# Optimization experiments

Measured on AMD Instinct MI355X. Metric: run time of the kernel, lower is better.

Reference implementation:

```python
import jax, jax.numpy as jnp
import numpy as np


def setup_inputs() -> dict:
    key = jax.random.key(0)
    k1, k2, k3 = jax.random.split(key, 3)
    B, D_IN, HIDDEN = 4096, 1024, 32768  # hidden = d_in * scale_size(32)
    x = jax.random.normal(k1, (B, D_IN), dtype=jnp.float32)
    W_enc = jax.random.normal(k2, (HIDDEN, D_IN), dtype=jnp.float32) * (1.0 / np.sqrt(D_IN))
    b_enc = jnp.zeros((HIDDEN,), dtype=jnp.float32)  # encoder.bias.data.zero_()
    # W_dec = encoder.weight.clone() then unit-norm rows (set_decoder_norm_to_unit_norm)
    W_dec = jax.random.normal(k3, (HIDDEN, D_IN), dtype=jnp.float32)
    W_dec = W_dec / (jnp.linalg.norm(W_dec, axis=1, keepdims=True) + jnp.finfo(jnp.float32).eps)
    b_dec = jnp.zeros((D_IN,), dtype=jnp.float32)
    return {"x": x, "W_enc": W_enc, "b_enc": b_enc, "W_dec": W_dec, "b_dec": b_dec, "k": 32}


def reference(x, W_enc, b_enc, W_dec, b_dec, k):
    # sae_in = x - b_dec; pre_acts = relu(encoder(sae_in))
    sae_in = x - b_dec
    pre_acts = jax.nn.relu(jnp.einsum('bd,hd->bh', sae_in, W_enc) + b_enc)  # [B, H]
    # topk_activation: keep top-k per row, zero elsewhere, then z @ W_dec.
    # Equivalent sparse decode: gather the k rows of W_dec and contract.
    topk_vals, topk_idx = jax.lax.top_k(pre_acts, k)  # [B, k]
    # x_reconstructed = z @ W_dec + b_dec  (z is the dense scatter of topk)
    x_rec = jnp.einsum('bk,bkd->bd', topk_vals, W_dec[topk_idx]) + b_dec
    return x_rec
```

## Files before the change

### kernel.cpp

```cpp
#include <hip/hip_runtime.h>
#include <hip/hip_bf16.h>
#include <stdint.h>
#include <stddef.h>


#define BROWS 4096
#define DIN   1024
#define HID   32768
#define KTOP  32
#define KC    48
#define PT    16

#define BM 256
#define BN 256
#define BK 64
#define NT (DIN / BK)
#define EP 264

typedef short short8_t __attribute__((ext_vector_type(8)));
typedef float fx4 __attribute__((ext_vector_type(4)));

__device__ __forceinline__ unsigned short f2bf(float f) {
  unsigned u = __float_as_uint(f);
  u += 0x7FFFu + ((u >> 16) & 1u);
  return (unsigned short)(u >> 16);
}

__global__ __launch_bounds__(256) void conv_wc(const float* __restrict__ W,
                                               unsigned short* __restrict__ Wbc, int c0) {
  int base = (blockIdx.x * 256 + threadIdx.x) * 4;
  float4 v = *(const float4*)(W + (size_t)c0 * DIN + base);
  ushort4 o;
  o.x = f2bf(v.x); o.y = f2bf(v.y); o.z = f2bf(v.z); o.w = f2bf(v.w);
  *(ushort4*)(Wbc + base) = o;
}

__global__ __launch_bounds__(256) void prep_x(const float* __restrict__ x,
                                              const float* __restrict__ bdec,
                                              unsigned short* __restrict__ xbf) {
  int base = (blockIdx.x * 256 + threadIdx.x) * 4;
  int col = base & (DIN - 1);
  float4 xv = *(const float4*)(x + base);
  float4 bv = *(const float4*)(bdec + col);
  ushort4 o;
  o.x = f2bf(xv.x - bv.x); o.y = f2bf(xv.y - bv.y);
  o.z = f2bf(xv.z - bv.z); o.w = f2bf(xv.w - bv.w);
  *(ushort4*)(xbf + base) = o;
}

__global__ __launch_bounds__(256) void init_cand(unsigned* __restrict__ cand) {
  int i = blockIdx.x * 256 + threadIdx.x;
  if (i < BROWS * KC) cand[i] = 0u;
}


__device__ __forceinline__ void stage_half(const unsigned short* __restrict__ g0,
                                           unsigned short* l0, int t, int k0) {
  const int w6 = (t >> 6) << 6;
#pragma unroll
  for (int i = 0; i < 2; ++i) {
    const int l  = i * 512 + t;
    const int r  = l >> 3;
    const int cl = (l & 7) ^ (r & 7);
    const unsigned short* g = g0 + (size_t)r * DIN + k0 + cl * 8;
    unsigned short* ld = l0 + (size_t)(i * 512 + w6) * 8;
    __builtin_amdgcn_global_load_lds((const __attribute__((address_space(1))) unsigned int*)g,
                                     (__attribute__((address_space(3))) unsigned int*)ld,
                                     16, 0, 0);
  }
}

__device__ __forceinline__ void tile_step(int tt,
                                          const unsigned short* __restrict__ Ab,
                                          const unsigned short* __restrict__ Wb,
                                          unsigned short* bc, unsigned short* bn,
                                          fx4 (&acc)[8][4],
                                          int t, int l16, int quad, int wm, int wn) {
  const int k1 = (tt + 1) * BK;
  const int k2 = (tt + 2) * BK;
  if (tt < NT - 1) { asm volatile("s_waitcnt vmcnt(4)" ::: "memory"); }
  else             { asm volatile("s_waitcnt vmcnt(0)" ::: "memory"); }
  __builtin_amdgcn_s_barrier();

  const unsigned short* Ar = bc + wm * 8192;
  const unsigned short* Br = bc + 16384 + (wn * 64 + l16) * 64;
  const int xs = l16 & 7;
  short8_t a[8], b0, b1;

#pragma unroll
  for (int mt = 0; mt < 8; ++mt)
    a[mt] = *(const short8_t*)(Ar + (mt * 16 + l16) * 64 + ((quad ^ xs) * 8));
  b0 = *(const short8_t*)(Br + 0 * 1024 + ((quad ^ xs) * 8));
  b1 = *(const short8_t*)(Br + 1 * 1024 + ((quad ^ xs) * 8));
  if (tt + 1 < NT) stage_half(Wb, bn + 16384, t, k1);
  __builtin_amdgcn_s_barrier();
  __builtin_amdgcn_s_setprio(1);
#pragma unroll
  for (int mt = 0; mt < 8; ++mt)
    acc[mt][0] = __builtin_amdgcn_mfma_f32_16x16x32_bf16(a[mt], b0, acc[mt][0], 0, 0, 0);
#pragma unroll
  for (int mt = 0; mt < 8; ++mt)
    acc[mt][1] = __builtin_amdgcn_mfma_f32_16x16x32_bf16(a[mt], b1, acc[mt][1], 0, 0, 0);
  __builtin_amdgcn_s_setprio(0);
  __builtin_amdgcn_s_barrier();

  b0 = *(const short8_t*)(Br + 2 * 1024 + ((quad ^ xs) * 8));
  b1 = *(const short8_t*)(Br + 3 * 1024 + ((quad ^ xs) * 8));
  if (tt + 1 < NT) stage_half(Wb + 128 * DIN, bn + 24576, t, k1);
  __builtin_amdgcn_s_barrier();
  __builtin_amdgcn_s_setprio(1);
#pragma unroll
  for (int mt = 0; mt < 8; ++mt)
    acc[mt][2] = __builtin_amdgcn_mfma_f32_16x16x32_bf16(a[mt], b0, acc[mt][2], 0, 0, 0);
#pragma unroll
  for (int mt = 0; mt < 8; ++mt)
    acc[mt][3] = __builtin_amdgcn_mfma_f32_16x16x32_bf16(a[mt], b1, acc[mt][3], 0, 0, 0);
  __builtin_amdgcn_s_setprio(0);
  __builtin_amdgcn_s_barrier();

#pragma unroll
  for (int mt = 0; mt < 8; ++mt)
    a[mt] = *(const short8_t*)(Ar + (mt * 16 + l16) * 64 + (((4 + quad) ^ xs) * 8));
  b0 = *(const short8_t*)(Br + 0 * 1024 + (((4 + quad) ^ xs) * 8));
  b1 = *(const short8_t*)(Br + 1 * 1024 + (((4 + quad) ^ xs) * 8));
  __builtin_amdgcn_s_barrier();
  __builtin_amdgcn_s_setprio(1);
#pragma unroll
  for (int mt = 0; mt < 8; ++mt)
    acc[mt][0] = __builtin_amdgcn_mfma_f32_16x16x32_bf16(a[mt], b0, acc[mt][0], 0, 0, 0);
#pragma unroll
  for (int mt = 0; mt < 8; ++mt)
    acc[mt][1] = __builtin_amdgcn_mfma_f32_16x16x32_bf16(a[mt], b1, acc[mt][1], 0, 0, 0);
  __builtin_amdgcn_s_setprio(0);
  __builtin_amdgcn_s_barrier();

  b0 = *(const short8_t*)(Br + 2 * 1024 + (((4 + quad) ^ xs) * 8));
  b1 = *(const short8_t*)(Br + 3 * 1024 + (((4 + quad) ^ xs) * 8));
  if (tt + 2 < NT) {
    stage_half(Ab,             bc,        t, k2);
    stage_half(Ab + 128 * DIN, bc + 8192, t, k2);
  }
  __builtin_amdgcn_s_barrier();
  __builtin_amdgcn_s_setprio(1);
#pragma unroll
  for (int mt = 0; mt < 8; ++mt)
    acc[mt][2] = __builtin_amdgcn_mfma_f32_16x16x32_bf16(a[mt], b0, acc[mt][2], 0, 0, 0);
#pragma unroll
  for (int mt = 0; mt < 8; ++mt)
    acc[mt][3] = __builtin_amdgcn_mfma_f32_16x16x32_bf16(a[mt], b1, acc[mt][3], 0, 0, 0);
  __builtin_amdgcn_s_setprio(0);
  __builtin_amdgcn_s_barrier();
}

__global__ __launch_bounds__(512, 2) void gemm_scores(
    const unsigned short* __restrict__ A,
    const unsigned short* __restrict__ W,
    const float* __restrict__ benc,
    unsigned short* __restrict__ scores,
    int Hc, int c0) {
  extern __shared__ unsigned short lds[];
  const int t    = threadIdx.x;
  const int lane = t & 63;
  const int wv   = t >> 6;
  const int wm   = wv >> 2;
  const int wn   = wv & 3;
  const int l16  = lane & 15;
  const int quad = lane >> 4;

  const int nwg  = (int)(gridDim.x * gridDim.y);
  const int orig = (int)(blockIdx.y * gridDim.x + blockIdx.x);
  const int q    = nwg >> 3, r8 = nwg & 7;
  const int xcd  = orig & 7, loc = orig >> 3;
  const int swz  = (xcd < r8 ? xcd * (q + 1) : r8 * (q + 1) + (xcd - r8) * q) + loc;
  const int bx   = swz % (int)gridDim.x;
  const int by   = swz / (int)gridDim.x;

  const int row0  = by * BM;
  const int colc0 = bx * BN;
  const unsigned short* Ab = A + (size_t)row0 * DIN;
  const unsigned short* Wb = W + (size_t)colc0 * DIN;

  unsigned short* buf0 = lds;
  unsigned short* buf1 = lds + 32768;

  fx4 acc[8][4];
  fx4 zero = {0.f, 0.f, 0.f, 0.f};
#pragma unroll
  for (int i = 0; i < 8; ++i)
#pragma unroll
    for (int j = 0; j < 4; ++j) acc[i][j] = zero;

  stage_half(Ab,            buf0,         t, 0);
  stage_half(Ab + 128*DIN,  buf0 + 8192,  t, 0);
  stage_half(Wb,            buf0 + 16384, t, 0);
  stage_half(Wb + 128*DIN,  buf0 + 24576, t, 0);
  stage_half(Ab,            buf1,         t, BK);
  stage_half(Ab + 128*DIN,  buf1 + 8192,  t, BK);

#pragma unroll 1
  for (int it = 0; it < NT / 2; ++it) {
    tile_step(2 * it,     Ab, Wb, buf0, buf1, acc, t, l16, quad, wm, wn);
    tile_step(2 * it + 1, Ab, Wb, buf1, buf0, acc, t, l16, quad, wm, wn);
  }

  const int colbase = colc0 + wn * 64;
  float bval[4];
#pragma unroll
  for (int nt = 0; nt < 4; ++nt) bval[nt] = benc[c0 + colbase + nt * 16 + l16];

  unsigned short* et = lds;
#pragma unroll
  for (int c = 0; c < 2; ++c) {
    __syncthreads();
    if (wm == c) {
#pragma unroll
      for (int nt = 0; nt < 4; ++nt) {
        const int col = wn * 64 + nt * 16 + l16;
#pragma unroll
        for (int mt = 0; mt < 8; ++mt)
#pragma unroll
          for (int rg = 0; rg < 4; ++rg) {
            const int row = mt * 16 + quad * 4 + rg;
            float v = acc[mt][nt][rg] + bval[nt];
            et[row * EP + col] = f2bf(v > 0.f ? v : 0.f);
          }
      }
    }
    __syncthreads();
    {
      const int row = t >> 2;
      const size_t gro = (size_t)(row0 + c * 128 + row) * Hc + colc0;
#pragma unroll
      for (int i = 0; i < 8; ++i) {
        const int ch = (t & 3) * 8 + i;
        short8_t v = *(const short8_t*)(et + row * EP + ch * 8);
        *(short8_t*)(scores + gro + ch * 8) = v;
      }
    }
  }
}

__global__ __launch_bounds__(128) void topk_cand(const unsigned short* __restrict__ scores,
                                                 int Hc, int c0,
                                                 unsigned* __restrict__ cand) {
  __shared__ unsigned lk[128 * 17];
  const int row = blockIdx.x;
  const int t = threadIdx.x;
  unsigned s[PT];
#pragma unroll
  for (int j = 0; j < PT; ++j) s[j] = 0u;

  const unsigned short* srow = scores + (size_t)row * Hc;
  for (int cb = t * 8; cb < Hc; cb += 128 * 8) {
    short8_t v = *(const short8_t*)(srow + cb);
    int gcb = c0 + cb;
#pragma unroll
    for (int e = 0; e < 8; ++e) {
      unsigned val = (unsigned)(unsigned short)v[e];
      unsigned key = (val << 16) | (unsigned)(0x7FFF - (gcb + e));
      if (key > s[PT - 1]) {
        unsigned prev = 0xFFFFFFFFu;
#pragma unroll
        for (int j = 0; j < PT; ++j) {
          unsigned sj = s[j];
          s[j] = (sj >= key) ? sj : (prev < key ? prev : key);
          prev = sj;
        }
      }
    }
  }
  if (t < KC) {
    unsigned key = cand[row * KC + t];
    if (key > s[PT - 1]) {
      unsigned prev = 0xFFFFFFFFu;
#pragma unroll
      for (int j = 0; j < PT; ++j) {
        unsigned sj = s[j];
        s[j] = (sj >= key) ? sj : (prev < key ? prev : key);
        prev = sj;
      }
    }
  }
#pragma unroll
  for (int j = 0; j < PT; ++j) lk[t * 17 + j] = s[j];
  __syncthreads();

  if (t < 64) {
    unsigned k0 = lk[t * 17];
    unsigned k1 = lk[(t + 64) * 17];
    int h0 = 0, h1 = 0;
    unsigned mywin = 0;
    for (int it = 0; it < KC; ++it) {
      unsigned wmax = (k0 > k1) ? k0 : k1;
#pragma unroll
      for (int off = 32; off >= 1; off >>= 1) {
        unsigned o = __shfl_down(wmax, (unsigned)off);
        if (o > wmax) wmax = o;
      }
      wmax = __shfl(wmax, 0);
      if (it == t) mywin = wmax;
      if (k0 == wmax)      { ++h0; k0 = (h0 < PT) ? lk[t * 17 + h0] : 0u; }
      else if (k1 == wmax) { ++h1; k1 = (h1 < PT) ? lk[(t + 64) * 17 + h1] : 0u; }
    }
    if (t < KC) cand[row * KC + t] = mywin;
  }
}

__global__ __launch_bounds__(256) void rescore_decode(
    const unsigned* __restrict__ cand,
    const float* __restrict__ x, const float* __restrict__ Wenc,
    const float* __restrict__ benc,
    const float* __restrict__ Wdec, const float* __restrict__ bdec,
    float* __restrict__ out) {
  __shared__ float xr[DIN];
  __shared__ double sc[KC];
  __shared__ int   scol[KC];
  __shared__ float fv[KTOP];
  __shared__ int   fi[KTOP];
  const int row = blockIdx.x, t = threadIdx.x;

  {
    float4 xv = *(const float4*)(x + (size_t)row * DIN + t * 4);
    float4 bv = *(const float4*)(bdec + t * 4);
    *(float4*)(xr + t * 4) = make_float4(xv.x - bv.x, xv.y - bv.y, xv.z - bv.z, xv.w - bv.w);
  }
  if (t < KC) scol[t] = 0x7FFF - (int)(cand[row * KC + t] & 0xFFFFu);
  if (t < KTOP) { fv[t] = 0.f; fi[t] = 0; }
  __syncthreads();

  const int wave = t >> 6, lane = t & 63;
  for (int j = wave; j < KC; j += 4) {
    int col = scol[j];
    const float* wr = Wenc + (size_t)col * DIN;
    double p = 0.0;
#pragma unroll
    for (int q = 0; q < 4; ++q) {
      int o = q * 256 + lane * 4;
      float4 w = *(const float4*)(wr + o);
      float4 xv = *(const float4*)(xr + o);
      p += (double)xv.x * (double)w.x + (double)xv.y * (double)w.y +
           (double)xv.z * (double)w.z + (double)xv.w * (double)w.w;
    }
#pragma unroll
    for (int off = 32; off >= 1; off >>= 1) p += __shfl_down(p, off);
    if (lane == 0) {
      double v = p + (double)benc[col];
      sc[j] = v > 0.0 ? v : 0.0;
    }
  }
  __syncthreads();

  if (t < KC) {
    double mv = sc[t];
    int mc = scol[t];
    int rank = 0;
    for (int j = 0; j < KC; ++j) {
      double oj = sc[j];
      if (oj > mv || (oj == mv && (scol[j] < mc || (scol[j] == mc && j < t)))) ++rank;
    }
    if (rank < KTOP) { fv[rank] = (float)mv; fi[rank] = mc; }
  }
  __syncthreads();

  const int c = t * 4;
  float4 bd = *(const float4*)(bdec + c);
  float a0 = bd.x, a1 = bd.y, a2 = bd.z, a3 = bd.w;
#pragma unroll 8
  for (int j = 0; j < KTOP; ++j) {
    float v = fv[j];
    float4 w = *(const float4*)(Wdec + (size_t)fi[j] * DIN + c);
    a0 += v * w.x; a1 += v * w.y; a2 += v * w.z; a3 += v * w.w;
  }
  *(float4*)(out + (size_t)row * DIN + c) = make_float4(a0, a1, a2, a3);
}

extern "C" void kernel_launch(void* const* d_in, const int* in_sizes, int n_in,
                              void* d_out, int out_size, void* d_ws, size_t ws_size,
                              hipStream_t stream) {
  const float* x    = (const float*)d_in[0];
  const float* Wenc = (const float*)d_in[1];
  const float* benc = (const float*)d_in[2];
  const float* Wdec = (const float*)d_in[3];
  const float* bdec = (const float*)d_in[4];
  float* out = (float*)d_out;

  char* ws = (char*)d_ws;
  unsigned short* xbf  = (unsigned short*)ws;
  unsigned*       cand = (unsigned*)(ws + (8u << 20));

  const size_t fixed = (size_t)(9u << 20);
  int Hc = HID;
  while (Hc > 256 &&
         fixed + (size_t)Hc * DIN * 2 + (size_t)BROWS * Hc * 2 > ws_size)
    Hc >>= 1;

  unsigned short* Wbc    = (unsigned short*)(ws + fixed);
  unsigned short* scores = (unsigned short*)(ws + fixed + (size_t)Hc * DIN * 2);

  static bool attr_set = false;
  if (!attr_set) {
    (void)hipFuncSetAttribute((const void*)gemm_scores,
                              hipFuncAttributeMaxDynamicSharedMemorySize, 131072);
    attr_set = true;
  }

  prep_x<<<BROWS * DIN / 1024, 256, 0, stream>>>(x, bdec, xbf);
  init_cand<<<(BROWS * KC + 255) / 256, 256, 0, stream>>>(cand);
  for (int c0 = 0; c0 < HID; c0 += Hc) {
    conv_wc<<<Hc, 256, 0, stream>>>(Wenc, Wbc, c0);
    gemm_scores<<<dim3(Hc / BN, BROWS / BM), 512, 131072, stream>>>(xbf, Wbc, benc, scores, Hc, c0);
    topk_cand<<<BROWS, 128, 0, stream>>>(scores, Hc, c0, cand);
  }
  rescore_decode<<<BROWS, 256, 0, stream>>>(cand, x, Wenc, benc, Wdec, bdec, out);
}
```

Baseline: 1.020 ms.

## Restructure GEMM tile step into 2x2 register-blocked MFMA quadrants with fewer barriers

```diff
diff --git a/kernel.cpp b/kernel.cpp
--- a/kernel.cpp
+++ b/kernel.cpp
@@ -54,20 +54,14 @@
 }
 
 
-__device__ __forceinline__ void stage_half(const unsigned short* __restrict__ g0,
-                                           unsigned short* l0, int t, int k0) {
-  const int w6 = (t >> 6) << 6;
-#pragma unroll
-  for (int i = 0; i < 2; ++i) {
-    const int l  = i * 512 + t;
-    const int r  = l >> 3;
-    const int cl = (l & 7) ^ (r & 7);
-    const unsigned short* g = g0 + (size_t)r * DIN + k0 + cl * 8;
-    unsigned short* ld = l0 + (size_t)(i * 512 + w6) * 8;
-    __builtin_amdgcn_global_load_lds((const __attribute__((address_space(1))) unsigned int*)g,
-                                     (__attribute__((address_space(3))) unsigned int*)ld,
-                                     16, 0, 0);
-  }
+__device__ __forceinline__ void stage_pair(const unsigned short* __restrict__ g,
+                                           unsigned short* l0, int voff, int w8) {
+  __builtin_amdgcn_global_load_lds((const __attribute__((address_space(1))) unsigned int*)(g + voff),
+                                   (__attribute__((address_space(3))) unsigned int*)(l0 + w8),
+                                   16, 0, 0);
+  __builtin_amdgcn_global_load_lds((const __attribute__((address_space(1))) unsigned int*)(g + voff + 64 * DIN),
+                                   (__attribute__((address_space(3))) unsigned int*)(l0 + w8 + 4096),
+                                   16, 0, 0);
 }
 
 __device__ __forceinline__ void tile_step(int tt,
@@ -75,81 +69,68 @@
                                           const unsigned short* __restrict__ Wb,
                                           unsigned short* bc, unsigned short* bn,
                                           fx4 (&acc)[8][4],
-                                          int t, int l16, int quad, int wm, int wn) {
-  const int k1 = (tt + 1) * BK;
-  const int k2 = (tt + 2) * BK;
+                                          int voff, int w8, int l16, int quad, int wm, int wn) {
   if (tt < NT - 1) { asm volatile("s_waitcnt vmcnt(4)" ::: "memory"); }
   else             { asm volatile("s_waitcnt vmcnt(0)" ::: "memory"); }
   __builtin_amdgcn_s_barrier();
 
-  const unsigned short* Ar = bc + wm * 8192;
+  const unsigned short* Ar = bc + wm * 8192 + l16 * 64;
   const unsigned short* Br = bc + 16384 + (wn * 64 + l16) * 64;
   const int xs = l16 & 7;
-  short8_t a[8], b0, b1;
-
-#pragma unroll
-  for (int mt = 0; mt < 8; ++mt)
-    a[mt] = *(const short8_t*)(Ar + (mt * 16 + l16) * 64 + ((quad ^ xs) * 8));
-  b0 = *(const short8_t*)(Br + 0 * 1024 + ((quad ^ xs) * 8));
-  b1 = *(const short8_t*)(Br + 1 * 1024 + ((quad ^ xs) * 8));
-  if (tt + 1 < NT) stage_half(Wb, bn + 16384, t, k1);
+  const int o0 = (quad ^ xs) * 8;
+  const int o1 = ((4 + quad) ^ xs) * 8;
+
+  short8_t aP[4], aQ[4], bP[4], bQ[4];
+#pragma unroll
+  for (int i = 0; i < 4; ++i) aP[i] = *(const short8_t*)(Ar + i * 1024 + o0);
+#pragma unroll
+  for (int i = 0; i < 4; ++i) bP[i] = *(const short8_t*)(Br + i * 1024 + o0);
+  if (tt + 1 < NT) {
+    stage_pair(Wb + (tt + 1) * BK,             bn + 16384, voff, w8);
+    stage_pair(Wb + 128 * DIN + (tt + 1) * BK, bn + 24576, voff, w8);
+  }
+#pragma unroll
+  for (int i = 0; i < 4; ++i) aQ[i] = *(const short8_t*)(Ar + (4 + i) * 1024 + o0);
+  __builtin_amdgcn_s_setprio(1);
+#pragma unroll
+  for (int i = 0; i < 4; ++i)
+#pragma unroll
+    for (int nt = 0; nt < 4; ++nt)
+      acc[i][nt] = __builtin_amdgcn_mfma_f32_16x16x32_bf16(aP[i], bP[nt], acc[i][nt], 0, 0, 0);
+  __builtin_amdgcn_s_setprio(0);
+
+#pragma unroll
+  for (int i = 0; i < 4; ++i) aP[i] = *(const short8_t*)(Ar + i * 1024 + o1);
+#pragma unroll
+  for (int i = 0; i < 4; ++i) bQ[i] = *(const short8_t*)(Br + i * 1024 + o1);
+  __builtin_amdgcn_s_setprio(1);
+#pragma unroll
+  for (int i = 0; i < 4; ++i)
+#pragma unroll
+    for (int nt = 0; nt < 4; ++nt)
+      acc[4 + i][nt] = __builtin_amdgcn_mfma_f32_16x16x32_bf16(aQ[i], bP[nt], acc[4 + i][nt], 0, 0, 0);
+  __builtin_amdgcn_s_setprio(0);
+
+#pragma unroll
+  for (int i = 0; i < 4; ++i) aQ[i] = *(const short8_t*)(Ar + (4 + i) * 1024 + o1);
+  __builtin_amdgcn_s_setprio(1);
+#pragma unroll
+  for (int i = 0; i < 4; ++i)
+#pragma unroll
+    for (int nt = 0; nt < 4; ++nt)
+      acc[i][nt] = __builtin_amdgcn_mfma_f32_16x16x32_bf16(aP[i], bQ[nt], acc[i][nt], 0, 0, 0);
+#pragma unroll
+  for (int i = 0; i < 4; ++i)
+#pragma unroll
+    for (int nt = 0; nt < 4; ++nt)
+      acc[4 + i][nt] = __builtin_amdgcn_mfma_f32_16x16x32_bf16(aQ[i], bQ[nt], acc[4 + i][nt], 0, 0, 0);
+  __builtin_amdgcn_s_setprio(0);
+
   __builtin_amdgcn_s_barrier();
-  __builtin_amdgcn_s_setprio(1);
-#pragma unroll
-  for (int mt = 0; mt < 8; ++mt)
-    acc[mt][0] = __builtin_amdgcn_mfma_f32_16x16x32_bf16(a[mt], b0, acc[mt][0], 0, 0, 0);
-#pragma unroll
-  for (int mt = 0; mt < 8; ++mt)
-    acc[mt][1] = __builtin_amdgcn_mfma_f32_16x16x32_bf16(a[mt], b1, acc[mt][1], 0, 0, 0);
-  __builtin_amdgcn_s_setprio(0);
-  __builtin_amdgcn_s_barrier();
-
-  b0 = *(const short8_t*)(Br + 2 * 1024 + ((quad ^ xs) * 8));
-  b1 = *(const short8_t*)(Br + 3 * 1024 + ((quad ^ xs) * 8));
-  if (tt + 1 < NT) stage_half(Wb + 128 * DIN, bn + 24576, t, k1);
-  __builtin_amdgcn_s_barrier();
-  __builtin_amdgcn_s_setprio(1);
-#pragma unroll
-  for (int mt = 0; mt < 8; ++mt)
-    acc[mt][2] = __builtin_amdgcn_mfma_f32_16x16x32_bf16(a[mt], b0, acc[mt][2], 0, 0, 0);
-#pragma unroll
-  for (int mt = 0; mt < 8; ++mt)
-    acc[mt][3] = __builtin_amdgcn_mfma_f32_16x16x32_bf16(a[mt], b1, acc[mt][3], 0, 0, 0);
-  __builtin_amdgcn_s_setprio(0);
-  __builtin_amdgcn_s_barrier();
-
-#pragma unroll
-  for (int mt = 0; mt < 8; ++mt)
-    a[mt] = *(const short8_t*)(Ar + (mt * 16 + l16) * 64 + (((4 + quad) ^ xs) * 8));
-  b0 = *(const short8_t*)(Br + 0 * 1024 + (((4 + quad) ^ xs) * 8));
-  b1 = *(const short8_t*)(Br + 1 * 1024 + (((4 + quad) ^ xs) * 8));
-  __builtin_amdgcn_s_barrier();
-  __builtin_amdgcn_s_setprio(1);
-#pragma unroll
-  for (int mt = 0; mt < 8; ++mt)
-    acc[mt][0] = __builtin_amdgcn_mfma_f32_16x16x32_bf16(a[mt], b0, acc[mt][0], 0, 0, 0);
-#pragma unroll
-  for (int mt = 0; mt < 8; ++mt)
-    acc[mt][1] = __builtin_amdgcn_mfma_f32_16x16x32_bf16(a[mt], b1, acc[mt][1], 0, 0, 0);
-  __builtin_amdgcn_s_setprio(0);
-  __builtin_amdgcn_s_barrier();
-
-  b0 = *(const short8_t*)(Br + 2 * 1024 + (((4 + quad) ^ xs) * 8));
-  b1 = *(const short8_t*)(Br + 3 * 1024 + (((4 + quad) ^ xs) * 8));
   if (tt + 2 < NT) {
-    stage_half(Ab,             bc,        t, k2);
-    stage_half(Ab + 128 * DIN, bc + 8192, t, k2);
-  }
-  __builtin_amdgcn_s_barrier();
-  __builtin_amdgcn_s_setprio(1);
-#pragma unroll
-  for (int mt = 0; mt < 8; ++mt)
-    acc[mt][2] = __builtin_amdgcn_mfma_f32_16x16x32_bf16(a[mt], b0, acc[mt][2], 0, 0, 0);
-#pragma unroll
-  for (int mt = 0; mt < 8; ++mt)
-    acc[mt][3] = __builtin_amdgcn_mfma_f32_16x16x32_bf16(a[mt], b1, acc[mt][3], 0, 0, 0);
-  __builtin_amdgcn_s_setprio(0);
-  __builtin_amdgcn_s_barrier();
+    stage_pair(Ab + (tt + 2) * BK,             bc,        voff, w8);
+    stage_pair(Ab + 128 * DIN + (tt + 2) * BK, bc + 8192, voff, w8);
+  }
 }
 
 __global__ __launch_bounds__(512, 2) void gemm_scores(
@@ -167,13 +148,14 @@
   const int l16  = lane & 15;
   const int quad = lane >> 4;
 
-  const int nwg  = (int)(gridDim.x * gridDim.y);
-  const int orig = (int)(blockIdx.y * gridDim.x + blockIdx.x);
+  const int gx   = (int)gridDim.x, gy = (int)gridDim.y;
+  const int nwg  = gx * gy;
+  const int orig = (int)blockIdx.x * gy + (int)blockIdx.y;
   const int q    = nwg >> 3, r8 = nwg & 7;
   const int xcd  = orig & 7, loc = orig >> 3;
   const int swz  = (xcd < r8 ? xcd * (q + 1) : r8 * (q + 1) + (xcd - r8) * q) + loc;
-  const int bx   = swz % (int)gridDim.x;
-  const int by   = swz / (int)gridDim.x;
+  const int bx   = swz / gy;
+  const int by   = swz % gy;
 
   const int row0  = by * BM;
   const int colc0 = bx * BN;
@@ -183,6 +165,10 @@
   unsigned short* buf0 = lds;
   unsigned short* buf1 = lds + 32768;
 
+  const int r_   = t >> 3;
+  const int voff = r_ * DIN + ((t & 7) ^ (r_ & 7)) * 8;
+  const int w8   = (t & ~63) * 8;
+
   fx4 acc[8][4];
   fx4 zero = {0.f, 0.f, 0.f, 0.f};
 #pragma unroll
@@ -190,17 +176,17 @@
 #pragma unroll
     for (int j = 0; j < 4; ++j) acc[i][j] = zero;
 
-  stage_half(Ab,            buf0,         t, 0);
-  stage_half(Ab + 128*DIN,  buf0 + 8192,  t, 0);
-  stage_half(Wb,            buf0 + 16384, t, 0);
-  stage_half(Wb + 128*DIN,  buf0 + 24576, t, 0);
-  stage_half(Ab,            buf1,         t, BK);
-  stage_half(Ab + 128*DIN,  buf1 + 8192,  t, BK);
+  stage_pair(Ab,                 buf0,         voff, w8);
+  stage_pair(Ab + 128 * DIN,     buf0 + 8192,  voff, w8);
+  stage_pair(Wb,                 buf0 + 16384, voff, w8);
+  stage_pair(Wb + 128 * DIN,     buf0 + 24576, voff, w8);
+  stage_pair(Ab + BK,            buf1,         voff, w8);
+  stage_pair(Ab + 128 * DIN + BK, buf1 + 8192, voff, w8);
 
 #pragma unroll 1
   for (int it = 0; it < NT / 2; ++it) {
-    tile_step(2 * it,     Ab, Wb, buf0, buf1, acc, t, l16, quad, wm, wn);
-    tile_step(2 * it + 1, Ab, Wb, buf1, buf0, acc, t, l16, quad, wm, wn);
+    tile_step(2 * it,     Ab, Wb, buf0, buf1, acc, voff, w8, l16, quad, wm, wn);
+    tile_step(2 * it + 1, Ab, Wb, buf1, buf0, acc, voff, w8, l16, quad, wm, wn);
   }
 
   const int colbase = colc0 + wn * 64;
```

Measured after the change: 1.001 ms. No clear change (-1.8%).
